# Kernel tuning notes

Hardware: AMD Instinct MI355X
Metric: run time of the kernel (lower is better)

The kernel has to match this reference:

```python
import jax, jax.numpy as jnp
import numpy as np

SOS_TOKEN_ID = 1
SUMMARY_LEN = 16  # decoder produces SUMMARY_LEN - 1 steps


def setup_inputs() -> dict:
    key = jax.random.key(0)
    ks = jax.random.split(key, 10)
    B, L, D, Vc, Vs = 256, 200, 512, 50000, 20000
    s = 0.05  # keep activations in a sane range for tanh/softmax
    return {
        "method_code": jax.random.randint(ks[0], (B, L), 0, Vc),
        "code_emb_table": jax.random.normal(ks[1], (Vc, D), jnp.float32) * s,
        "summary_emb_table": jax.random.normal(ks[2], (Vs, D), jnp.float32) * s,
        "w_ih": jax.random.normal(ks[3], (4 * D, D), jnp.float32) * s,
        "w_hh": jax.random.normal(ks[4], (4 * D, D), jnp.float32) * s,
        "b_ih": jnp.zeros((4 * D,), jnp.float32),
        "b_hh": jnp.zeros((4 * D,), jnp.float32),
        "t_w": jax.random.normal(ks[5], (D, D), jnp.float32) * s,
        "t_b": jnp.zeros((D,), jnp.float32),
        "h_w": jax.random.normal(ks[6], (D, D), jnp.float32) * s,
        "h_b": jnp.zeros((D,), jnp.float32),
        "p_w": jax.random.normal(ks[7], (Vs, D), jnp.float32) * s,
        "p_b": jnp.zeros((Vs,), jnp.float32),
    }


def reference(method_code, code_emb_table, summary_emb_table,
              w_ih, w_hh, b_ih, b_hh, t_w, t_b, h_w, h_b, p_w, p_b):
    B = method_code.shape[0]
    D = code_emb_table.shape[1]
    code_emb = code_emb_table[method_code]  # [B, L, D]

    def step(carry, _):
        h, c, prev_tok = carry
        x = summary_emb_table[prev_tok]                       # [B, D]
        # torch LSTMCell: gates ordered i, f, g, o
        gates = x @ w_ih.T + b_ih + h @ w_hh.T + b_hh          # [B, 4D]
        i_g, f_g, g_g, o_g = jnp.split(gates, 4, axis=-1)
        c_new = jax.nn.sigmoid(f_g) * c + jax.nn.sigmoid(i_g) * jnp.tanh(g_g)
        h_new = jax.nn.sigmoid(o_g) * jnp.tanh(c_new)
        # dot-product attention over code embeddings
        attn = jax.nn.softmax(jnp.einsum('bd,bld->bl', h_new, code_emb), axis=-1)
        t = jnp.einsum('bl,bld->bd', attn, code_emb)           # [B, D]
        pre = t @ t_w.T + t_b + h_new @ h_w.T + h_b            # [B, D]
        logits = jnp.tanh(pre) @ p_w.T + p_b                   # [B, V]
        next_tok = jnp.argmax(logits, axis=-1)                 # greedy feedback
        return (h_new, c_new, next_tok), logits

    h0 = jnp.zeros((B, D), code_emb.dtype)
    c0 = jnp.zeros((B, D), code_emb.dtype)
    prev0 = jnp.full((B,), SOS_TOKEN_ID, dtype=method_code.dtype)
    _, logits_seq = jax.lax.scan(step, (h0, c0, prev0), None, length=SUMMARY_LEN - 1)
    return jnp.transpose(logits_seq, (1, 0, 2))  # [B, summary_len-1, V]
```

## Files before the change

### kernel.cpp

```cpp
#include <hip/hip_runtime.h>
#include <math.h>

#define BB 256
#define LL 200
#define DD 512
#define VS 20000
#define VS_PAD 20224
#define STEPS 15

typedef __attribute__((ext_vector_type(8))) short bf16x8;
typedef __attribute__((ext_vector_type(4))) float f32x4;

__device__ __forceinline__ unsigned int mono_key(float f) {
    unsigned int u = __float_as_uint(f);
    return (u & 0x80000000u) ? ~u : (u | 0x80000000u);
}

__device__ __forceinline__ unsigned short f2bf_rn(float x) {
    unsigned int u = __float_as_uint(x);
    unsigned int r = (u + 0x7FFFu + ((u >> 16) & 1u)) >> 16;
    return (unsigned short)r;
}
__device__ __forceinline__ float bf2f(unsigned short b) {
    return __uint_as_float((unsigned int)b << 16);
}

__device__ __forceinline__ void split_store8(float4 v0, float4 v1,
    unsigned short* __restrict__ hi, unsigned short* __restrict__ lo)
{
    ushort4 h0, h1, l0, l1;
    h0.x = f2bf_rn(v0.x); l0.x = f2bf_rn(v0.x - bf2f(h0.x));
    h0.y = f2bf_rn(v0.y); l0.y = f2bf_rn(v0.y - bf2f(h0.y));
    h0.z = f2bf_rn(v0.z); l0.z = f2bf_rn(v0.z - bf2f(h0.z));
    h0.w = f2bf_rn(v0.w); l0.w = f2bf_rn(v0.w - bf2f(h0.w));
    h1.x = f2bf_rn(v1.x); l1.x = f2bf_rn(v1.x - bf2f(h1.x));
    h1.y = f2bf_rn(v1.y); l1.y = f2bf_rn(v1.y - bf2f(h1.y));
    h1.z = f2bf_rn(v1.z); l1.z = f2bf_rn(v1.z - bf2f(h1.z));
    h1.w = f2bf_rn(v1.w); l1.w = f2bf_rn(v1.w - bf2f(h1.w));
    *(ushort4*)hi = h0; *(ushort4*)(hi + 4) = h1;
    *(ushort4*)lo = l0; *(ushort4*)(lo + 4) = l1;
}

__device__ __forceinline__ void split_frag(float4 v0, float4 v1, bf16x8& hi, bf16x8& lo)
{
    float vv[8] = {v0.x, v0.y, v0.z, v0.w, v1.x, v1.y, v1.z, v1.w};
    #pragma unroll
    for (int j = 0; j < 8; j++) {
        unsigned short hb = f2bf_rn(vv[j]);
        hi[j] = (short)hb;
        lo[j] = (short)f2bf_rn(vv[j] - bf2f(hb));
    }
}

__global__ __launch_bounds__(256) void init_keys_kernel(unsigned long long* keys) {
    keys[threadIdx.x] = (unsigned long long)(unsigned int)(~1u);
}


__global__ __launch_bounds__(256) void split_pw_kernel(
    const float* __restrict__ p_w, unsigned short* __restrict__ p_hi,
    unsigned short* __restrict__ p_lo)
{
    size_t q = (size_t)blockIdx.x * 256 + threadIdx.x;
    int P   = (int)(q >> 10);
    int rem = (int)(q & 1023);
    int c   = rem >> 6;
    int l   = rem & 63;
    int row = P * 16 + (l & 15);
    int ks  = c * 32 + (l >> 4) * 8;
    float4 v0 = {0.f, 0.f, 0.f, 0.f}, v1 = {0.f, 0.f, 0.f, 0.f};
    if (row < VS) {
        const float* src = p_w + (size_t)row * DD + ks;
        v0 = *(const float4*)src;
        v1 = *(const float4*)(src + 4);
    }
    split_store8(v0, v1, p_hi + q * 8, p_lo + q * 8);
}

template <int PERM>
__global__ __launch_bounds__(256) void split_wcat_kernel(
    const float* __restrict__ s0, const float* __restrict__ s1,
    unsigned short* __restrict__ wh, unsigned short* __restrict__ wl)
{
    size_t q = (size_t)blockIdx.x * 256 + threadIdx.x;
    int P   = (int)(q >> 11);
    int rem = (int)(q & 2047);
    int c   = rem >> 6;
    int l   = rem & 63;
    int row;
    if (PERM) row = (P & 3) * 512 + (P >> 2) * 16 + (l & 15);
    else      row = P * 16 + (l & 15);
    int k   = c * 32 + (l >> 4) * 8;
    const float* src = (k < 512) ? (s0 + (size_t)row * DD + k)
                                 : (s1 + (size_t)row * DD + (k - 512));
    float4 v0 = *(const float4*)src;
    float4 v1 = *(const float4*)(src + 4);
    split_store8(v0, v1, wh + q * 8, wl + q * 8);
}

__global__ __launch_bounds__(256) void gates_lstm_kernel(
    const float* __restrict__ sum_emb, const unsigned long long* __restrict__ keys,
    const unsigned short* __restrict__ hin_hi, const unsigned short* __restrict__ hin_lo,
    const unsigned short* __restrict__ w1h, const unsigned short* __restrict__ w1l,
    const float* __restrict__ bi, const float* __restrict__ bh,
    float* __restrict__ c, float* __restrict__ h,
    unsigned short* __restrict__ hout_hi, unsigned short* __restrict__ hout_lo)
{
    const int tid  = threadIdx.x;
    const int lane = tid & 63;
    const int wav  = tid >> 6;
    const int col = lane & 15;
    const int kg  = lane >> 4;
    const int m0  = (blockIdx.y * 4 + wav) * 16;
    const int nt  = blockIdx.x;

    unsigned int tok = ~(unsigned int)(keys[m0 + col] & 0xFFFFFFFFull);

    const size_t ahoff = (size_t)(m0 >> 4) * 8192 + (size_t)lane * 8;
    const size_t boff  = (size_t)(nt * 4) * 16384 + (size_t)lane * 8;

    f32x4 acc[4];
    #pragma unroll
    for (int g = 0; g < 4; g++) acc[g] = (f32x4){0.f, 0.f, 0.f, 0.f};

    bf16x8 fa_h[2], fa_l[2], fb_h[2][4], fb_l[2][4];

#define GL_LOAD(C, BUF)                                                            \
    {                                                                              \
        if ((C) < 16) {                                                            \
            const float* s_ = sum_emb + (size_t)tok * DD + (C) * 32 + kg * 8;      \
            float4 v0 = *(const float4*)s_;                                        \
            float4 v1 = *(const float4*)(s_ + 4);                                  \
            split_frag(v0, v1, fa_h[BUF], fa_l[BUF]);                              \
        } else {                                                                   \
            fa_h[BUF] = *(const bf16x8*)(hin_hi + ahoff + ((C) - 16) * 512);       \
            fa_l[BUF] = *(const bf16x8*)(hin_lo + ahoff + ((C) - 16) * 512);       \
        }                                                                          \
        _Pragma("unroll")                                                          \
        for (int g = 0; g < 4; g++) {                                              \
            fb_h[BUF][g] = *(const bf16x8*)(w1h + boff + (size_t)g * 16384 + (C) * 512); \
            fb_l[BUF][g] = *(const bf16x8*)(w1l + boff + (size_t)g * 16384 + (C) * 512); \
        }                                                                          \
    }

    GL_LOAD(0, 0);
    #pragma unroll
    for (int cc = 0; cc < 32; cc++) {
        const int cur = cc & 1, nxt = cur ^ 1;
        if (cc < 31) GL_LOAD(cc + 1, nxt);
        #pragma unroll
        for (int g = 0; g < 4; g++) {
            acc[g] = __builtin_amdgcn_mfma_f32_16x16x32_bf16(fa_h[cur], fb_h[cur][g], acc[g], 0, 0, 0);
            acc[g] = __builtin_amdgcn_mfma_f32_16x16x32_bf16(fa_h[cur], fb_l[cur][g], acc[g], 0, 0, 0);
            acc[g] = __builtin_amdgcn_mfma_f32_16x16x32_bf16(fa_l[cur], fb_h[cur][g], acc[g], 0, 0, 0);
        }
    }
#undef GL_LOAD

    const int feat = nt * 16 + col;
    float bias[4];
    #pragma unroll
    for (int g = 0; g < 4; g++)
        bias[g] = bi[g * 512 + feat] + bh[g * 512 + feat];

    #pragma unroll
    for (int r = 0; r < 4; r++) {
        const int b = m0 + kg * 4 + r;
        float vi = acc[0][r] + bias[0];
        float vf = acc[1][r] + bias[1];
        float vg = acc[2][r] + bias[2];
        float vo = acc[3][r] + bias[3];
        double ig = 1.0 / (1.0 + exp(-(double)vi));
        double fg = 1.0 / (1.0 + exp(-(double)vf));
        double gv = tanh((double)vg);
        double og = 1.0 / (1.0 + exp(-(double)vo));
        size_t cidx = (size_t)b * DD + feat;
        double cn = fg * (double)c[cidx] + ig * gv;
        double hn = og * tanh(cn);
        c[cidx] = (float)cn;
        float hf = (float)hn;
        h[cidx] = hf;
        size_t hidx = (size_t)(b >> 4) * 8192 + (size_t)(feat >> 5) * 512
                    + (size_t)(((feat >> 3) & 3) * 16 + (b & 15)) * 8 + (feat & 7);
        unsigned short hb2 = f2bf_rn(hf);
        hout_hi[hidx] = hb2;
        hout_lo[hidx] = f2bf_rn(hf - bf2f(hb2));
    }
}

__global__ __launch_bounds__(256) void pre_kernel(
    const unsigned short* __restrict__ t_hi, const unsigned short* __restrict__ t_lo,
    const unsigned short* __restrict__ h_hi, const unsigned short* __restrict__ h_lo,
    const unsigned short* __restrict__ w2h, const unsigned short* __restrict__ w2l,
    const float* __restrict__ tb, const float* __restrict__ hbv,
    unsigned short* __restrict__ o_hi, unsigned short* __restrict__ o_lo)
{
    const int tid  = threadIdx.x;
    const int lane = tid & 63;
    const int wav  = tid >> 6;
    const int col  = lane & 15;
    const int kg   = lane >> 4;
    const int m0   = blockIdx.y * 16;
    const int n0   = blockIdx.x * 32;

    const unsigned short* ah = (wav < 2) ? t_hi : h_hi;
    const unsigned short* al = (wav < 2) ? t_lo : h_lo;
    const size_t aoff = (size_t)(m0 >> 4) * 8192 + (size_t)lane * 8
                      + (size_t)((wav & 1) * 8) * 512;
    const size_t boff = (size_t)(n0 >> 4) * 16384 + (size_t)lane * 8
                      + (size_t)(wav * 8) * 512;

    f32x4 acc[2];
    acc[0] = (f32x4){0.f, 0.f, 0.f, 0.f};
    acc[1] = (f32x4){0.f, 0.f, 0.f, 0.f};

    bf16x8 fa_h[2], fa_l[2], fb_h[2][2], fb_l[2][2];
    fa_h[0] = *(const bf16x8*)(ah + aoff);
    fa_l[0] = *(const bf16x8*)(al + aoff);
    #pragma unroll
    for (int g = 0; g < 2; g++) {
        fb_h[0][g] = *(const bf16x8*)(w2h + boff + (size_t)g * 16384);
        fb_l[0][g] = *(const bf16x8*)(w2l + boff + (size_t)g * 16384);
    }
    #pragma unroll
    for (int cc = 0; cc < 8; cc++) {
        const int cur = cc & 1, nxt = cur ^ 1;
        if (cc < 7) {
            const int off = (cc + 1) * 512;
            fa_h[nxt] = *(const bf16x8*)(ah + aoff + off);
            fa_l[nxt] = *(const bf16x8*)(al + aoff + off);
            #pragma unroll
            for (int g = 0; g < 2; g++) {
                fb_h[nxt][g] = *(const bf16x8*)(w2h + boff + (size_t)g * 16384 + off);
                fb_l[nxt][g] = *(const bf16x8*)(w2l + boff + (size_t)g * 16384 + off);
            }
        }
        #pragma unroll
        for (int g = 0; g < 2; g++) {
            acc[g] = __builtin_amdgcn_mfma_f32_16x16x32_bf16(fa_h[cur], fb_h[cur][g], acc[g], 0, 0, 0);
            acc[g] = __builtin_amdgcn_mfma_f32_16x16x32_bf16(fa_h[cur], fb_l[cur][g], acc[g], 0, 0, 0);
            acc[g] = __builtin_amdgcn_mfma_f32_16x16x32_bf16(fa_l[cur], fb_h[cur][g], acc[g], 0, 0, 0);
        }
    }

    __shared__ float psum[4][16][32];
    #pragma unroll
    for (int g = 0; g < 2; g++)
        #pragma unroll
        for (int r = 0; r < 4; r++)
            psum[wav][kg * 4 + r][g * 16 + col] = acc[g][r];
    __syncthreads();

    #pragma unroll
    for (int e = 0; e < 2; e++) {
        const int idx  = tid * 2 + e;
        const int row  = idx >> 5, coln = idx & 31;
        const int b    = m0 + row;
        const int n    = n0 + coln;
        float accs = (psum[0][row][coln] + psum[1][row][coln])
                   + (psum[2][row][coln] + psum[3][row][coln]);
        float val = accs + (tb[n] + hbv[n]);
        float v2 = (float)tanh((double)val);
        int P = b >> 4, colb = b & 15;
        int cc2 = n >> 5, kgg = (n >> 3) & 3, jj = n & 7;
        size_t oidx = (size_t)P * 8192 + (size_t)cc2 * 512
                    + (size_t)(kgg * 16 + colb) * 8 + jj;
        unsigned short hb = f2bf_rn(v2);
        o_hi[oidx] = hb;
        o_lo[oidx] = f2bf_rn(v2 - bf2f(hb));
    }
}

template <int NCH, int EPI, int WPB>
__global__ __launch_bounds__(64 * WPB, 3) void mfma_gemm(
    const unsigned short* __restrict__ a0h, const unsigned short* __restrict__ a0l,
    const unsigned short* __restrict__ a1h, const unsigned short* __restrict__ a1l,
    const unsigned short* __restrict__ bmh, const unsigned short* __restrict__ bml,
    const float* __restrict__ bias0, const float* __restrict__ bias1,
    float* __restrict__ outp,
    unsigned short* __restrict__ o_hi, unsigned short* __restrict__ o_lo,
    unsigned long long* __restrict__ keys, int s)
{
    const int tid  = threadIdx.x;
    const int lane = tid & 63;
    const int wav  = tid >> 6;
    const int col = lane & 15;
    const int kg  = lane >> 4;
    const int m0 = (blockIdx.y * WPB + wav) * 32;
    const int n0 = blockIdx.x * 64;

    const size_t aoff = (size_t)(m0 >> 4) * 8192 + (size_t)lane * 8;
    const size_t boff = (size_t)(n0 >> 4) * (NCH * 512) + (size_t)lane * 8;

    f32x4 acc[2][4];
    #pragma unroll
    for (int f = 0; f < 2; f++)
        #pragma unroll
        for (int g = 0; g < 4; g++)
            acc[f][g] = (f32x4){0.f, 0.f, 0.f, 0.f};

    bf16x8 fah[2][2], fal[2][2], fbh[2][4], fbl[2][4];

#define LOAD_CHUNK(C, BUF)                                                         \
    {                                                                              \
        const unsigned short* ah_ = ((NCH == 16) || ((C) < 16)) ? a0h : a1h;       \
        const unsigned short* al_ = ((NCH == 16) || ((C) < 16)) ? a0l : a1l;       \
        const int cc_ = (C) & 15;                                                  \
        _Pragma("unroll")                                                          \
        for (int f = 0; f < 2; f++) {                                              \
            fah[BUF][f] = *(const bf16x8*)(ah_ + aoff + (size_t)f * 8192 + cc_ * 512); \
            fal[BUF][f] = *(const bf16x8*)(al_ + aoff + (size_t)f * 8192 + cc_ * 512); \
        }                                                                          \
        _Pragma("unroll")                                                          \
        for (int g = 0; g < 4; g++) {                                              \
            fbh[BUF][g] = *(const bf16x8*)(bmh + boff + (size_t)g * (NCH * 512) + (C) * 512); \
            fbl[BUF][g] = *(const bf16x8*)(bml + boff + (size_t)g * (NCH * 512) + (C) * 512); \
        }                                                                          \
    }

    LOAD_CHUNK(0, 0);
    #pragma unroll
    for (int c = 0; c < NCH; c++) {
        const int cur = c & 1, nxt = cur ^ 1;
        if (c < NCH - 1) LOAD_CHUNK(c + 1, nxt);
        #pragma unroll
        for (int f = 0; f < 2; f++)
            #pragma unroll
            for (int g = 0; g < 4; g++) {
                acc[f][g] = __builtin_amdgcn_mfma_f32_16x16x32_bf16(fah[cur][f], fbh[cur][g], acc[f][g], 0, 0, 0);
                acc[f][g] = __builtin_amdgcn_mfma_f32_16x16x32_bf16(fah[cur][f], fbl[cur][g], acc[f][g], 0, 0, 0);
                acc[f][g] = __builtin_amdgcn_mfma_f32_16x16x32_bf16(fal[cur][f], fbh[cur][g], acc[f][g], 0, 0, 0);
            }
    }
#undef LOAD_CHUNK

    float bias[4];
    #pragma unroll
    for (int g = 0; g < 4; g++) {
        int v = n0 + g * 16 + col;
        bias[g] = (v < VS) ? bias0[v] : 0.f;
    }

    #pragma unroll
    for (int f = 0; f < 2; f++) {
        #pragma unroll
        for (int r = 0; r < 4; r++) {
            const int b = m0 + f * 16 + kg * 4 + r;
            float* orow = outp + ((size_t)b * STEPS + s) * VS;
            unsigned long long kmax = 0ull;
            #pragma unroll
            for (int g = 0; g < 4; g++) {
                int v = n0 + g * 16 + col;
                float val = acc[f][g][r] + bias[g];
                if (v < VS) {
                    orow[v] = val;
                    unsigned long long key =
                        ((unsigned long long)mono_key(val) << 32) |
                        (unsigned long long)(unsigned int)(~v);
                    if (key > kmax) kmax = key;
                }
            }
            #pragma unroll
            for (int mk = 1; mk < 16; mk <<= 1) {
                unsigned long long o = __shfl_xor(kmax, mk, 64);
                if (o > kmax) kmax = o;
            }
            if (col == 0) {
                if (kmax > *(volatile unsigned long long*)&keys[b])
                    atomicMax(&keys[b], kmax);
            }
        }
    }
}

__global__ __launch_bounds__(512) void attn_kernel(
    const int* __restrict__ method_code, const float* __restrict__ code_emb,
    const float* __restrict__ h, unsigned short* __restrict__ t_hi,
    unsigned short* __restrict__ t_lo, unsigned long long* __restrict__ keys)
{
    const int b = blockIdx.x;
    const int tid = threadIdx.x;
    const int lane = tid & 63, wave = tid >> 6;

    __shared__ float sc[LL];
    __shared__ int   rows[LL];
    __shared__ float fred[256];
    __shared__ double dred[256];
    __shared__ float ts[DD];
    __shared__ float part[8][DD];

    if (tid < LL) rows[tid] = method_code[b * LL + tid];
    if (tid == 0) keys[b] = 0ull;
    const float* hb = h + (size_t)b * DD;
    float4 h0 = *(const float4*)(hb + lane * 8);
    float4 h1 = *(const float4*)(hb + lane * 8 + 4);
    __syncthreads();

    for (int l = wave; l < LL; l += 8) {
        const float* e = code_emb + (size_t)rows[l] * DD + lane * 8;
        float4 e0 = *(const float4*)e;
        float4 e1 = *(const float4*)(e + 4);
        float p = h0.x * e0.x + h0.y * e0.y + h0.z * e0.z + h0.w * e0.w
                + h1.x * e1.x + h1.y * e1.y + h1.z * e1.z + h1.w * e1.w;
        #pragma unroll
        for (int m = 1; m < 64; m <<= 1) p += __shfl_xor(p, m, 64);
        if (lane == 0) sc[l] = p;
    }
    __syncthreads();

    if (tid < 256) fred[tid] = (tid < LL) ? sc[tid] : -INFINITY;
    __syncthreads();
    for (int s2 = 128; s2 > 0; s2 >>= 1) {
        if (tid < s2) fred[tid] = fmaxf(fred[tid], fred[tid + s2]);
        __syncthreads();
    }
    float smax = fred[0];
    __syncthreads();
    double w = (tid < LL) ? exp((double)sc[tid] - (double)smax) : 0.0;
    if (tid < 256) dred[tid] = w;
    __syncthreads();
    for (int s2 = 128; s2 > 0; s2 >>= 1) {
        if (tid < s2) dred[tid] += dred[tid + s2];
        __syncthreads();
    }
    double ssum = dred[0];
    __syncthreads();
    if (tid < LL) sc[tid] = (float)(w / ssum);
    __syncthreads();

    float pa[8] = {0.f, 0.f, 0.f, 0.f, 0.f, 0.f, 0.f, 0.f};
    for (int l = wave; l < LL; l += 8) {
        float wl = sc[l];
        const float* e = code_emb + (size_t)rows[l] * DD + lane * 8;
        float4 e0 = *(const float4*)e;
        float4 e1 = *(const float4*)(e + 4);
        pa[0] = fmaf(wl, e0.x, pa[0]); pa[1] = fmaf(wl, e0.y, pa[1]);
        pa[2] = fmaf(wl, e0.z, pa[2]); pa[3] = fmaf(wl, e0.w, pa[3]);
        pa[4] = fmaf(wl, e1.x, pa[4]); pa[5] = fmaf(wl, e1.y, pa[5]);
        pa[6] = fmaf(wl, e1.z, pa[6]); pa[7] = fmaf(wl, e1.w, pa[7]);
    }
    #pragma unroll
    for (int j = 0; j < 8; j++) part[wave][lane * 8 + j] = pa[j];
    __syncthreads();

    {
        const int d = tid;
        float v01 = part[0][d] + part[1][d];
        float v23 = part[2][d] + part[3][d];
        float v45 = part[4][d] + part[5][d];
        float v67 = part[6][d] + part[7][d];
        ts[d] = (v01 + v23) + (v45 + v67);
    }
    __syncthreads();

    if (tid < 64) {
        const int cc = tid >> 2, kgg = tid & 3;
        const float* src = ts + cc * 32 + kgg * 8;
        float4 v0 = *(const float4*)src;
        float4 v1 = *(const float4*)(src + 4);
        size_t base = (size_t)(b >> 4) * 8192 + (size_t)cc * 512
                    + (size_t)(kgg * 16 + (b & 15)) * 8;
        split_store8(v0, v1, t_hi + base, t_lo + base);
    }
}

extern "C" void kernel_launch(void* const* d_in, const int* in_sizes, int n_in,
                              void* d_out, int out_size, void* d_ws, size_t ws_size,
                              hipStream_t stream)
{
    const int*   method_code = (const int*)d_in[0];
    const float* code_emb    = (const float*)d_in[1];
    const float* sum_emb     = (const float*)d_in[2];
    const float* w_ih        = (const float*)d_in[3];
    const float* w_hh        = (const float*)d_in[4];
    const float* b_ih        = (const float*)d_in[5];
    const float* b_hh        = (const float*)d_in[6];
    const float* t_w         = (const float*)d_in[7];
    const float* t_b         = (const float*)d_in[8];
    const float* h_w         = (const float*)d_in[9];
    const float* h_b         = (const float*)d_in[10];
    const float* p_w         = (const float*)d_in[11];
    const float* p_b         = (const float*)d_in[12];
    float* out = (float*)d_out;

    float* h     = (float*)d_ws;
    float* c     = h + BB * DD;
    unsigned long long* keys = (unsigned long long*)(c + BB * DD);
    unsigned short* a_hi   = (unsigned short*)(keys + BB);
    unsigned short* a_lo   = a_hi   + BB * DD;
    unsigned short* t_hi   = a_lo   + BB * DD;
    unsigned short* t_lo   = t_hi   + BB * DD;
    unsigned short* hp0_hi = t_lo   + BB * DD;
    unsigned short* hp0_lo = hp0_hi + BB * DD;
    unsigned short* hp1_hi = hp0_lo + BB * DD;
    unsigned short* hp1_lo = hp1_hi + BB * DD;
    unsigned short* w1_hi  = hp1_lo + BB * DD;
    unsigned short* w1_lo  = w1_hi  + (size_t)2048 * 1024;
    unsigned short* w2_hi  = w1_lo  + (size_t)2048 * 1024;
    unsigned short* w2_lo  = w2_hi  + (size_t)512 * 1024;
    unsigned short* p_hi   = w2_lo  + (size_t)512 * 1024;
    unsigned short* p_lo   = p_hi   + (size_t)VS_PAD * DD;

    hipMemsetAsync(h, 0, (size_t)2 * BB * DD * sizeof(float), stream);
    hipMemsetAsync(hp0_hi, 0, (size_t)2 * BB * DD * sizeof(unsigned short), stream);
    init_keys_kernel<<<1, 256, 0, stream>>>(keys);
    split_pw_kernel<<<(VS_PAD * 64) / 256, 256, 0, stream>>>(p_w, p_hi, p_lo);
    split_wcat_kernel<1><<<1024, 256, 0, stream>>>(w_ih, w_hh, w1_hi, w1_lo);
    split_wcat_kernel<0><<<256, 256, 0, stream>>>(t_w, h_w, w2_hi, w2_lo);

    for (int s = 0; s < STEPS; s++) {
        const unsigned short* hin_hi  = (s & 1) ? hp1_hi : hp0_hi;
        const unsigned short* hin_lo  = (s & 1) ? hp1_lo : hp0_lo;
        unsigned short*       hout_hi = (s & 1) ? hp0_hi : hp1_hi;
        unsigned short*       hout_lo = (s & 1) ? hp0_lo : hp1_lo;

        gates_lstm_kernel<<<dim3(32, 4), 256, 0, stream>>>(
            sum_emb, keys, hin_hi, hin_lo, w1_hi, w1_lo, b_ih, b_hh,
            c, h, hout_hi, hout_lo);
        attn_kernel<<<256, 512, 0, stream>>>(method_code, code_emb, h, t_hi, t_lo, keys);
        pre_kernel<<<dim3(16, 16), 256, 0, stream>>>(
            t_hi, t_lo, hout_hi, hout_lo, w2_hi, w2_lo, t_b, h_b, a_hi, a_lo);
        mfma_gemm<16, 2, 4><<<dim3(316, 2), 256, 0, stream>>>(
            a_hi, a_lo, nullptr, nullptr, p_hi, p_lo, p_b, nullptr,
            out, nullptr, nullptr, keys, s);
    }
}
```

Measured before the change: 2.068 ms.

## Deepen B prefetch in logits GEMM, prefetch attention rows, shrink LSTM blocks

The logits GEMM now keeps three register buffers for the B (p_w) fragments so loads run two chunks ahead, and drops its occupancy hint from 3 to 2 to make room for the extra registers. The attention score and context loops software-prefetch the next code-embedding row before doing the current dot product or FMA. The gates/LSTM kernel launches twice as many 128-thread blocks, which spreads the work over more CUs. Together these aim to hide global-load latency, at the cost of higher register pressure and lower occupancy in the GEMM.

```diff
diff --git a/kernel.cpp b/kernel.cpp
--- a/kernel.cpp
+++ b/kernel.cpp
@@ -98,7 +98,7 @@
     split_store8(v0, v1, wh + q * 8, wl + q * 8);
 }
 
-__global__ __launch_bounds__(256) void gates_lstm_kernel(
+__global__ __launch_bounds__(128) void gates_lstm_kernel(
     const float* __restrict__ sum_emb, const unsigned long long* __restrict__ keys,
     const unsigned short* __restrict__ hin_hi, const unsigned short* __restrict__ hin_lo,
     const unsigned short* __restrict__ w1h, const unsigned short* __restrict__ w1l,
@@ -111,7 +111,7 @@
     const int wav  = tid >> 6;
     const int col = lane & 15;
     const int kg  = lane >> 4;
-    const int m0  = (blockIdx.y * 4 + wav) * 16;
+    const int m0  = (blockIdx.y * 2 + wav) * 16;
     const int nt  = blockIdx.x;
 
     unsigned int tok = ~(unsigned int)(keys[m0 + col] & 0xFFFFFFFFull);
@@ -272,7 +272,7 @@
 }
 
 template <int NCH, int EPI, int WPB>
-__global__ __launch_bounds__(64 * WPB, 3) void mfma_gemm(
+__global__ __launch_bounds__(64 * WPB, 2) void mfma_gemm(
     const unsigned short* __restrict__ a0h, const unsigned short* __restrict__ a0l,
     const unsigned short* __restrict__ a1h, const unsigned short* __restrict__ a1l,
     const unsigned short* __restrict__ bmh, const unsigned short* __restrict__ bml,
@@ -299,9 +299,10 @@
         for (int g = 0; g < 4; g++)
             acc[f][g] = (f32x4){0.f, 0.f, 0.f, 0.f};
 
-    bf16x8 fah[2][2], fal[2][2], fbh[2][4], fbl[2][4];
-
-#define LOAD_CHUNK(C, BUF)                                                         \
+    bf16x8 fah[2][2], fal[2][2];
+    bf16x8 fbh[3][4], fbl[3][4];
+
+#define LOAD_A(C, BUF)                                                             \
     {                                                                              \
         const unsigned short* ah_ = ((NCH == 16) || ((C) < 16)) ? a0h : a1h;       \
         const unsigned short* al_ = ((NCH == 16) || ((C) < 16)) ? a0l : a1l;       \
@@ -311,6 +312,9 @@
             fah[BUF][f] = *(const bf16x8*)(ah_ + aoff + (size_t)f * 8192 + cc_ * 512); \
             fal[BUF][f] = *(const bf16x8*)(al_ + aoff + (size_t)f * 8192 + cc_ * 512); \
         }                                                                          \
+    }
+#define LOAD_B(C, BUF)                                                             \
+    {                                                                              \
         _Pragma("unroll")                                                          \
         for (int g = 0; g < 4; g++) {                                              \
             fbh[BUF][g] = *(const bf16x8*)(bmh + boff + (size_t)g * (NCH * 512) + (C) * 512); \
@@ -318,21 +322,26 @@
         }                                                                          \
     }
 
-    LOAD_CHUNK(0, 0);
+    LOAD_B(0, 0);
+    LOAD_B(1, 1);
+    LOAD_A(0, 0);
     #pragma unroll
     for (int c = 0; c < NCH; c++) {
-        const int cur = c & 1, nxt = cur ^ 1;
-        if (c < NCH - 1) LOAD_CHUNK(c + 1, nxt);
+        const int bcur = c % 3;
+        const int acur = c & 1;
+        if (c + 2 < NCH) LOAD_B(c + 2, (c + 2) % 3);
+        if (c + 1 < NCH) LOAD_A(c + 1, (c + 1) & 1);
         #pragma unroll
         for (int f = 0; f < 2; f++)
             #pragma unroll
             for (int g = 0; g < 4; g++) {
-                acc[f][g] = __builtin_amdgcn_mfma_f32_16x16x32_bf16(fah[cur][f], fbh[cur][g], acc[f][g], 0, 0, 0);
-                acc[f][g] = __builtin_amdgcn_mfma_f32_16x16x32_bf16(fah[cur][f], fbl[cur][g], acc[f][g], 0, 0, 0);
-                acc[f][g] = __builtin_amdgcn_mfma_f32_16x16x32_bf16(fal[cur][f], fbh[cur][g], acc[f][g], 0, 0, 0);
-            }
-    }
-#undef LOAD_CHUNK
+                acc[f][g] = __builtin_amdgcn_mfma_f32_16x16x32_bf16(fah[acur][f], fbh[bcur][g], acc[f][g], 0, 0, 0);
+                acc[f][g] = __builtin_amdgcn_mfma_f32_16x16x32_bf16(fah[acur][f], fbl[bcur][g], acc[f][g], 0, 0, 0);
+                acc[f][g] = __builtin_amdgcn_mfma_f32_16x16x32_bf16(fal[acur][f], fbh[bcur][g], acc[f][g], 0, 0, 0);
+            }
+    }
+#undef LOAD_A
+#undef LOAD_B
 
     float bias[4];
     #pragma unroll
@@ -396,15 +405,24 @@
     float4 h1 = *(const float4*)(hb + lane * 8 + 4);
     __syncthreads();
 
-    for (int l = wave; l < LL; l += 8) {
-        const float* e = code_emb + (size_t)rows[l] * DD + lane * 8;
+    {
+        const float* e = code_emb + (size_t)rows[wave] * DD + lane * 8;
         float4 e0 = *(const float4*)e;
         float4 e1 = *(const float4*)(e + 4);
-        float p = h0.x * e0.x + h0.y * e0.y + h0.z * e0.z + h0.w * e0.w
-                + h1.x * e1.x + h1.y * e1.y + h1.z * e1.z + h1.w * e1.w;
-        #pragma unroll
-        for (int m = 1; m < 64; m <<= 1) p += __shfl_xor(p, m, 64);
-        if (lane == 0) sc[l] = p;
+        for (int l = wave; l < LL; l += 8) {
+            float4 n0v = e0, n1v = e1;
+            if (l + 8 < LL) {
+                const float* en = code_emb + (size_t)rows[l + 8] * DD + lane * 8;
+                n0v = *(const float4*)en;
+                n1v = *(const float4*)(en + 4);
+            }
+            float p = h0.x * e0.x + h0.y * e0.y + h0.z * e0.z + h0.w * e0.w
+                    + h1.x * e1.x + h1.y * e1.y + h1.z * e1.z + h1.w * e1.w;
+            #pragma unroll
+            for (int m = 1; m < 64; m <<= 1) p += __shfl_xor(p, m, 64);
+            if (lane == 0) sc[l] = p;
+            e0 = n0v; e1 = n1v;
+        }
     }
     __syncthreads();
 
@@ -429,15 +447,24 @@
     __syncthreads();
 
     float pa[8] = {0.f, 0.f, 0.f, 0.f, 0.f, 0.f, 0.f, 0.f};
-    for (int l = wave; l < LL; l += 8) {
-        float wl = sc[l];
-        const float* e = code_emb + (size_t)rows[l] * DD + lane * 8;
+    {
+        const float* e = code_emb + (size_t)rows[wave] * DD + lane * 8;
         float4 e0 = *(const float4*)e;
         float4 e1 = *(const float4*)(e + 4);
-        pa[0] = fmaf(wl, e0.x, pa[0]); pa[1] = fmaf(wl, e0.y, pa[1]);
-        pa[2] = fmaf(wl, e0.z, pa[2]); pa[3] = fmaf(wl, e0.w, pa[3]);
-        pa[4] = fmaf(wl, e1.x, pa[4]); pa[5] = fmaf(wl, e1.y, pa[5]);
-        pa[6] = fmaf(wl, e1.z, pa[6]); pa[7] = fmaf(wl, e1.w, pa[7]);
+        for (int l = wave; l < LL; l += 8) {
+            float4 n0v = e0, n1v = e1;
+            if (l + 8 < LL) {
+                const float* en = code_emb + (size_t)rows[l + 8] * DD + lane * 8;
+                n0v = *(const float4*)en;
+                n1v = *(const float4*)(en + 4);
+            }
+            float wl = sc[l];
+            pa[0] = fmaf(wl, e0.x, pa[0]); pa[1] = fmaf(wl, e0.y, pa[1]);
+            pa[2] = fmaf(wl, e0.z, pa[2]); pa[3] = fmaf(wl, e0.w, pa[3]);
+            pa[4] = fmaf(wl, e1.x, pa[4]); pa[5] = fmaf(wl, e1.y, pa[5]);
+            pa[6] = fmaf(wl, e1.z, pa[6]); pa[7] = fmaf(wl, e1.w, pa[7]);
+            e0 = n0v; e1 = n1v;
+        }
     }
     #pragma unroll
     for (int j = 0; j < 8; j++) part[wave][lane * 8 + j] = pa[j];
@@ -514,7 +541,7 @@
         unsigned short*       hout_hi = (s & 1) ? hp0_hi : hp1_hi;
         unsigned short*       hout_lo = (s & 1) ? hp0_lo : hp1_lo;
 
-        gates_lstm_kernel<<<dim3(32, 4), 256, 0, stream>>>(
+        gates_lstm_kernel<<<dim3(32, 8), 128, 0, stream>>>(
             sum_emb, keys, hin_hi, hin_lo, w1_hi, w1_lo, b_ih, b_hh,
             c, h, hout_hi, hout_lo);
         attn_kernel<<<256, 512, 0, stream>>>(method_code, code_emb, h, t_hi, t_lo, keys);
```

New measurement: 2.103 ms. No clear change (+1.7%).
